# Kernel tuning notes

Measured on AMD Instinct MI355X. Metric: run time of the kernel, lower is better.

## Reference

```python
import jax, jax.numpy as jnp
import numpy as np

B, SQ, SK, D, H, DK, DV = 4, 2048, 2048, 1024, 16, 64, 64


def setup_inputs() -> dict:
    key = jax.random.key(0)
    ks = jax.random.split(key, 12)

    def xav(k, shape):
        fan_in, fan_out = shape[-2], shape[-1]
        lim = (6.0 / (fan_in + fan_out)) ** 0.5
        return jax.random.uniform(k, shape, jnp.float32, -lim, lim)

    return {
        "Q": jax.random.normal(ks[0], (B, SQ, D), jnp.float32),
        "K": jax.random.normal(ks[1], (B, SK, D), jnp.float32),
        "V": jax.random.normal(ks[2], (B, SK, D), jnp.float32),
        "padding_mask": jnp.zeros((B, 1, SK), jnp.bool_),
        "Wq": xav(ks[3], (H, D, DK)),
        "bq": jnp.zeros((H, DK), jnp.float32),
        "Wk": xav(ks[4], (H, D, DK)),
        "bk": jnp.zeros((H, DK), jnp.float32),
        "Wv": xav(ks[5], (H, D, DV)),
        "bv": jnp.zeros((H, DV), jnp.float32),
        "Wo": xav(ks[6], (H, DV, DV)),   # per-head Attention.linear
        "bo": jnp.zeros((H, DV), jnp.float32),
        "Wf": xav(ks[7], (H * DV, D)),   # final MultiHeadAttention.linear
        "bf": jnp.zeros((D,), jnp.float32),
    }


def reference(Q, K, V, padding_mask, Wq, bq, Wk, bk, Wv, bv, Wo, bo, Wf, bf):
    # Per-head projections, batched over heads instead of a python loop.
    q = jnp.einsum("bsd,hdk->bhsk", Q, Wq) + bq[:, None, :]  # [B,H,SQ,DK]
    k = jnp.einsum("bsd,hdk->bhsk", K, Wk) + bk[:, None, :]  # [B,H,SK,DK]
    v = jnp.einsum("bsd,hdv->bhsv", V, Wv) + bv[:, None, :]  # [B,H,SK,DV]

    scale = float(DK) ** 0.5
    w = jnp.einsum("bhqd,bhkd->bhqk", q, k) / scale           # [B,H,SQ,SK]

    causal = jnp.triu(jnp.ones((SQ, SK), jnp.bool_), 1)       # masking=True path
    w = jnp.where(causal[None, None], -jnp.inf, w)
    w = jnp.where(padding_mask[:, None, :, :], -jnp.inf, w)   # [B,1,1,SK]

    score = jnp.nan_to_num(jax.nn.softmax(w, axis=-1))        # nan_to_num as in torch
    # dropout p=0.0 -> identity
    ctx = jnp.einsum("bhqk,bhkv->bhqv", score, v)             # [B,H,SQ,DV]
    heads = jnp.einsum("bhqv,hvu->bhqu", ctx, Wo) + bo[:, None, :]
    concat = heads.transpose(0, 2, 1, 3).reshape(B, SQ, H * DV)
    return concat @ Wf + bf
```

## Files before the change

### kernel.cpp

```cpp
#include <hip/hip_runtime.h>

typedef unsigned short u16;
typedef __attribute__((ext_vector_type(8))) short short8;
typedef __attribute__((ext_vector_type(4))) float f32x4;

#define NEG (-1e30f)
#define SCL 0.180336880f

#define WS_WPQ   (0u)
#define WS_WPK   (2u<<20)
#define WS_WPV   (4u<<20)
#define WS_WBIG  (6u<<20)
#define WS_BC    (8u<<20)
#define WS_QB    (9u<<20)
#define WS_KB    (25u<<20)
#define WS_VB    (41u<<20)
#define WS_QP    (57u<<20)
#define WS_KP    (73u<<20)
#define WS_VP    (89u<<20)
#define WS_VT    (105u<<20)
#define WS_CTX   (121u<<20)

__device__ __forceinline__ u16 f2b(float f) {
    union { float f; unsigned u; } x; x.f = f;
    unsigned r = x.u + 0x7fffu + ((x.u >> 16) & 1u);
    return (u16)(r >> 16);
}

__device__ __forceinline__ void gload16(const void* g, void* lds) {
    __builtin_amdgcn_global_load_lds(
        (const __attribute__((address_space(1))) void*)g,
        (__attribute__((address_space(3))) void*)lds, 16, 0, 0);
}

__global__ __launch_bounds__(256) void conv_bf16(const float* __restrict__ in,
                                                 u16* __restrict__ out) {
    unsigned i = blockIdx.x * 256u + threadIdx.x;
    const float4* p = (const float4*)(in + (size_t)i * 8);
    float4 a = p[0], b = p[1];
    short8 o;
    o[0]=(short)f2b(a.x); o[1]=(short)f2b(a.y); o[2]=(short)f2b(a.z); o[3]=(short)f2b(a.w);
    o[4]=(short)f2b(b.x); o[5]=(short)f2b(b.y); o[6]=(short)f2b(b.z); o[7]=(short)f2b(b.w);
    *(short8*)(out + (size_t)i * 8) = o;
}

__global__ __launch_bounds__(256) void pack_qkv(const float* __restrict__ Wq,
                                                const float* __restrict__ Wk,
                                                const float* __restrict__ Wv,
                                                u16* __restrict__ pq,
                                                u16* __restrict__ pk,
                                                u16* __restrict__ pv) {
    unsigned idx = blockIdx.x * 256u + threadIdx.x;
    unsigned n = idx >> 10, d = idx & 1023u;
    unsigned h = n >> 6, kk = n & 63u;
    unsigned src = (h * 1024u + d) * 64u + kk;
    pq[idx] = f2b(Wq[src]);
    pk[idx] = f2b(Wk[src]);
    pv[idx] = f2b(Wv[src]);
}

__global__ __launch_bounds__(256) void make_wbig(const float* __restrict__ Wo,
                                                 const float* __restrict__ Wf,
                                                 u16* __restrict__ wbig) {
    unsigned idx = blockIdx.x * 256u + threadIdx.x;
    unsigned n = idx >> 10, k = idx & 1023u;
    unsigned h = k >> 6;
    float s = 0.f;
#pragma unroll 8
    for (int u = 0; u < 64; ++u)
        s += Wo[k * 64u + u] * Wf[(h * 64u + u) * 1024u + n];
    wbig[(size_t)n * 1024u + k] = f2b(s);
}

__global__ __launch_bounds__(256) void make_bcomb(const float* __restrict__ bo,
                                                  const float* __restrict__ bf,
                                                  const float* __restrict__ Wf,
                                                  float* __restrict__ bc) {
    __shared__ float red[16][17];
    const int tx = threadIdx.x & 15, ty = threadIdx.x >> 4;
    const int n = blockIdx.x * 16 + tx;
    float s = 0.f;
#pragma unroll
    for (int i = 0; i < 64; ++i) {
        int x = ty * 64 + i;
        s += bo[x] * Wf[(size_t)x * 1024 + n];
    }
    red[ty][tx] = s;
    __syncthreads();
    if (ty == 0) {
        float t = bf[n];
#pragma unroll
        for (int y = 0; y < 16; ++y) t += red[y][tx];
        bc[n] = t;
    }
}

__global__ __launch_bounds__(256) void vtrans(const u16* __restrict__ vp,
                                              u16* __restrict__ vt) {
    const int kvt = blockIdx.x, bh = blockIdx.y, b = bh >> 4, h = bh & 15;
    const int tid = threadIdx.x;
    __shared__ u16 T[64][72];
    {
        int kv_r = tid >> 2, dg = (tid & 3) * 16;
        const u16* src = vp + ((size_t)(b * 2048 + kvt * 64 + kv_r)) * 1024 + h * 64 + dg;
        short8 x0 = *(const short8*)src;
        short8 x1 = *(const short8*)(src + 8);
#pragma unroll
        for (int i = 0; i < 8; ++i) { T[dg + i][kv_r] = (u16)x0[i]; T[dg + 8 + i][kv_r] = (u16)x1[i]; }
    }
    __syncthreads();
    {
        int dv = tid >> 2, cg = (tid & 3) * 16;
        int swz = (dv & 7) << 3;
        u16* dst = vt + ((size_t)(bh * 64 + dv)) * 2048 + kvt * 64;
#pragma unroll
        for (int q = 0; q < 2; ++q) {
            int c0 = cg + q * 8;
            short8 y;
#pragma unroll
            for (int i = 0; i < 8; ++i) y[i] = (short)T[dv][c0 + i];
            *(short8*)(dst + (c0 ^ swz)) = y;
        }
    }
}

template <int OUT_BF16>
__global__ __launch_bounds__(256) void gemm_bf16(const u16* __restrict__ A,
                                                 const u16* __restrict__ Bt,
                                                 const float* __restrict__ bias,
                                                 void* __restrict__ Cv,
                                                 int M, int N, int K) {
    __shared__ __align__(16) u16 As[128 * 64];
    __shared__ __align__(16) u16 Bs[128 * 64];
    const int tid = threadIdx.x;
    const int lane = tid & 63, w = tid >> 6;
    const int li = lane & 15, g = lane >> 4;
    const int bm = blockIdx.y * 128, bn = blockIdx.x * 128;
    const int wm = w >> 1, wn = w & 1;

    f32x4 acc[4][4];
#pragma unroll
    for (int m = 0; m < 4; ++m)
#pragma unroll
        for (int n = 0; n < 4; ++n) acc[m][n] = (f32x4){0.f, 0.f, 0.f, 0.f};

    for (int k0 = 0; k0 < K; k0 += 64) {
        __syncthreads();
#pragma unroll
        for (int r = 0; r < 4; ++r) {
            int ch  = (r * 4 + w) * 64 + lane;
            int row = ch >> 3;
            int ck  = (ch & 7) ^ (row & 7);
            gload16(A  + (size_t)(bm + row) * K + k0 + ck * 8, (char*)As + (r * 4 + w) * 1024);
            gload16(Bt + (size_t)(bn + row) * K + k0 + ck * 8, (char*)Bs + (r * 4 + w) * 1024);
        }
        __syncthreads();
#pragma unroll
        for (int kk = 0; kk < 2; ++kk) {
            short8 a[4], b[4];
#pragma unroll
            for (int m = 0; m < 4; ++m) {
                int row = wm * 64 + m * 16 + li;
                int c = (kk * 4 + g) ^ (row & 7);
                a[m] = *(const short8*)(As + row * 64 + c * 8);
            }
#pragma unroll
            for (int n = 0; n < 4; ++n) {
                int row = wn * 64 + n * 16 + li;
                int c = (kk * 4 + g) ^ (row & 7);
                b[n] = *(const short8*)(Bs + row * 64 + c * 8);
            }
#pragma unroll
            for (int m = 0; m < 4; ++m)
#pragma unroll
                for (int n = 0; n < 4; ++n)
                    acc[m][n] = __builtin_amdgcn_mfma_f32_16x16x32_bf16(a[m], b[n], acc[m][n], 0, 0, 0);
        }
    }

#pragma unroll
    for (int n = 0; n < 4; ++n) {
        int col = bn + wn * 64 + n * 16 + li;
        float bv = bias[col];
#pragma unroll
        for (int m = 0; m < 4; ++m)
#pragma unroll
            for (int j = 0; j < 4; ++j) {
                int row = bm + wm * 64 + m * 16 + g * 4 + j;
                float v = acc[m][n][j] + bv;
                if (OUT_BF16) ((u16*)Cv)[(size_t)row * N + col] = f2b(v);
                else          ((float*)Cv)[(size_t)row * N + col] = v;
            }
    }
}

__global__ __launch_bounds__(256) void flash_attn(const u16* __restrict__ qp,
                                                  const u16* __restrict__ kp,
                                                  const u16* __restrict__ vt,
                                                  const unsigned char* __restrict__ pmask,
                                                  u16* __restrict__ ctx) {
    const int bh = blockIdx.x, b = bh >> 4, h = bh & 15;
    const int qt = 31 - blockIdx.y;
    const int tid = threadIdx.x, lane = tid & 63, w = tid >> 6;
    const int li = lane & 15, g = lane >> 4;

    __shared__ __align__(16) u16 Ks[2][64 * 64];
    __shared__ __align__(16) u16 Vs[2][64 * 64];
    __shared__ __align__(16) u16 Ps[64 * 64];

    auto STAGE = [&](int buf, int kt) {
#pragma unroll
        for (int r = 0; r < 2; ++r) {
            int ch  = (r * 4 + w) * 64 + lane;
            int row = ch >> 3, cc = ch & 7;
            int ck  = cc ^ (row & 7);
            gload16(kp + (size_t)(b * 2048 + kt * 64 + row) * 1024 + h * 64 + ck * 8,
                    (char*)(Ks[buf]) + (r * 4 + w) * 1024);
            gload16(vt + (size_t)(bh * 64 + row) * 2048 + kt * 64 + cc * 8,
                    (char*)(Vs[buf]) + (r * 4 + w) * 1024);
        }
    };

    STAGE(0, 0);
    const int rq = w * 16 + li;
    const u16* qg = qp + (size_t)(b * 2048 + qt * 64 + rq) * 1024 + h * 64;
    short8 aq0 = *(const short8*)(qg + g * 8);
    short8 aq1 = *(const short8*)(qg + 32 + g * 8);

    float m_i[4], l_i[4];
    f32x4 o_acc[4];
#pragma unroll
    for (int j = 0; j < 4; ++j) { m_i[j] = NEG; l_i[j] = 0.f; }
#pragma unroll
    for (int n = 0; n < 4; ++n) o_acc[n] = (f32x4){0.f, 0.f, 0.f, 0.f};

    const unsigned char* pm = pmask + (size_t)b * 2048;

    __syncthreads();
    int cur = 0;

    for (int kt = 0; kt <= qt; ++kt) {
        if (kt < qt) STAGE(cur ^ 1, kt + 1);

        f32x4 s[4];
#pragma unroll
        for (int n = 0; n < 4; ++n) s[n] = (f32x4){0.f, 0.f, 0.f, 0.f};
        __builtin_amdgcn_s_setprio(1);
#pragma unroll
        for (int kk = 0; kk < 2; ++kk) {
            short8 aq = kk ? aq1 : aq0;
#pragma unroll
            for (int n = 0; n < 4; ++n) {
                int rk = n * 16 + li;
                short8 bk = *(const short8*)(Ks[cur] + rk * 64 + (((kk * 4 + g) ^ (li & 7))) * 8);
                s[n] = __builtin_amdgcn_mfma_f32_16x16x32_bf16(aq, bk, s[n], 0, 0, 0);
            }
        }
        __builtin_amdgcn_s_setprio(0);

        float mcol[4];
#pragma unroll
        for (int n = 0; n < 4; ++n) mcol[n] = pm[kt * 64 + n * 16 + li] ? NEG : 0.f;
        const bool diag = (kt == qt);
        float rmax[4];
#pragma unroll
        for (int j = 0; j < 4; ++j) rmax[j] = NEG;
#pragma unroll
        for (int n = 0; n < 4; ++n) {
            int colk = kt * 64 + n * 16 + li;
#pragma unroll
            for (int j = 0; j < 4; ++j) {
                int rowq = qt * 64 + w * 16 + g * 4 + j;
                float v = s[n][j] * SCL + mcol[n];
                if (diag && colk > rowq) v = NEG;
                s[n][j] = v;
                rmax[j] = fmaxf(rmax[j], v);
            }
        }
#pragma unroll
        for (int off = 1; off < 16; off <<= 1)
#pragma unroll
            for (int j = 0; j < 4; ++j)
                rmax[j] = fmaxf(rmax[j], __shfl_xor(rmax[j], off));

        bool grow = (rmax[0] > m_i[0]) | (rmax[1] > m_i[1]) |
                    (rmax[2] > m_i[2]) | (rmax[3] > m_i[3]);
        if (__any(grow)) {
#pragma unroll
            for (int j = 0; j < 4; ++j) {
                float mn = fmaxf(m_i[j], rmax[j]);
                float a  = exp2f(m_i[j] - mn);
                m_i[j] = mn;
                l_i[j] *= a;
#pragma unroll
                for (int n = 0; n < 4; ++n) o_acc[n][j] *= a;
            }
        }

        float p[4][4], rsum[4] = {0.f, 0.f, 0.f, 0.f};
#pragma unroll
        for (int n = 0; n < 4; ++n)
#pragma unroll
            for (int j = 0; j < 4; ++j) {
                float pv = exp2f(s[n][j] - m_i[j]);
                p[n][j] = pv;
                rsum[j] += pv;
            }
#pragma unroll
        for (int off = 1; off < 16; off <<= 1)
#pragma unroll
            for (int j = 0; j < 4; ++j)
                rsum[j] += __shfl_xor(rsum[j], off);
#pragma unroll
        for (int j = 0; j < 4; ++j) l_i[j] += rsum[j];

#pragma unroll
        for (int j = 0; j < 4; ++j) {
            int rl  = g * 4 + j;
            int rg  = w * 16 + rl;
            int swz = (rl & 7) << 3;
#pragma unroll
            for (int n = 0; n < 4; ++n)
                Ps[rg * 64 + ((n * 16 + li) ^ swz)] = f2b(p[n][j]);
        }

        __builtin_amdgcn_s_setprio(1);
#pragma unroll
        for (int kk = 0; kk < 2; ++kk) {
            short8 pa = *(const short8*)(Ps + rq * 64 + (((kk * 4 + g) ^ (li & 7))) * 8);
#pragma unroll
            for (int n = 0; n < 4; ++n) {
                int rv = n * 16 + li;
                short8 vb = *(const short8*)(Vs[cur] + rv * 64 + (((kk * 4 + g) ^ (li & 7))) * 8);
                o_acc[n] = __builtin_amdgcn_mfma_f32_16x16x32_bf16(pa, vb, o_acc[n], 0, 0, 0);
            }
        }
        __builtin_amdgcn_s_setprio(0);

        __syncthreads();
        cur ^= 1;
    }

    float inv[4];
#pragma unroll
    for (int j = 0; j < 4; ++j) inv[j] = 1.f / l_i[j];
#pragma unroll
    for (int n = 0; n < 4; ++n)
#pragma unroll
        for (int j = 0; j < 4; ++j) {
            int rowq = qt * 64 + w * 16 + g * 4 + j;
            ctx[(size_t)(b * 2048 + rowq) * 1024 + h * 64 + n * 16 + li] = f2b(o_acc[n][j] * inv[j]);
        }
}

extern "C" void kernel_launch(void* const* d_in, const int* in_sizes, int n_in,
                              void* d_out, int out_size, void* d_ws, size_t ws_size,
                              hipStream_t stream) {
    const float* Q  = (const float*)d_in[0];
    const float* K  = (const float*)d_in[1];
    const float* V  = (const float*)d_in[2];
    const unsigned char* pmask = (const unsigned char*)d_in[3];
    const float* Wq = (const float*)d_in[4];
    const float* bq = (const float*)d_in[5];
    const float* Wk = (const float*)d_in[6];
    const float* bk = (const float*)d_in[7];
    const float* Wv = (const float*)d_in[8];
    const float* bv = (const float*)d_in[9];
    const float* Wo = (const float*)d_in[10];
    const float* bo = (const float*)d_in[11];
    const float* Wf = (const float*)d_in[12];
    const float* bf = (const float*)d_in[13];
    float* out = (float*)d_out;
    char*  ws  = (char*)d_ws;

    u16* WPQ = (u16*)(ws + WS_WPQ);  u16* WPK = (u16*)(ws + WS_WPK);
    u16* WPV = (u16*)(ws + WS_WPV);  u16* WBG = (u16*)(ws + WS_WBIG);
    float* BC = (float*)(ws + WS_BC);
    u16* QB = (u16*)(ws + WS_QB);  u16* KB = (u16*)(ws + WS_KB);  u16* VB = (u16*)(ws + WS_VB);
    u16* QP = (u16*)(ws + WS_QP);  u16* KP = (u16*)(ws + WS_KP);  u16* VP = (u16*)(ws + WS_VP);
    u16* VT = (u16*)(ws + WS_VT);  u16* CTX = (u16*)(ws + WS_CTX);

    conv_bf16<<<4096, 256, 0, stream>>>(Q, QB);
    conv_bf16<<<4096, 256, 0, stream>>>(K, KB);
    conv_bf16<<<4096, 256, 0, stream>>>(V, VB);
    pack_qkv<<<4096, 256, 0, stream>>>(Wq, Wk, Wv, WPQ, WPK, WPV);
    make_wbig<<<4096, 256, 0, stream>>>(Wo, Wf, WBG);
    make_bcomb<<<64, 256, 0, stream>>>(bo, bf, Wf, BC);

    dim3 g1(8, 64);
    gemm_bf16<1><<<g1, 256, 0, stream>>>(QB, WPQ, bq, QP, 8192, 1024, 1024);
    gemm_bf16<1><<<g1, 256, 0, stream>>>(KB, WPK, bk, KP, 8192, 1024, 1024);
    gemm_bf16<1><<<g1, 256, 0, stream>>>(VB, WPV, bv, VP, 8192, 1024, 1024);

    vtrans<<<dim3(32, 64), 256, 0, stream>>>(VP, VT);

    flash_attn<<<dim3(64, 32), 256, 0, stream>>>(QP, KP, VT, pmask, CTX);

    gemm_bf16<0><<<g1, 256, 0, stream>>>(CTX, WBG, BC, out, 8192, 1024, 1024);
}
```

Measured before the change: 471.7 us.

## Double-buffer GEMM, restructure flash attention softmax, and speed up weight preprocessing

The projection GEMM now double-buffers its LDS tiles so the next k-tile loads while the current one computes, and the softmax scale is folded into the Q projection epilogue. Flash attention swaps the MFMA operands so each lane owns a whole query row. This drops most cross-lane max and sum reductions, and P is packed with v_cvt_pk_bf16_f32. The padding mask becomes a precomputed float bias with a per-batch any-padded flag so unpadded batches skip mask loads, and the diagonal tile is peeled out of the loop. The weight pack and Wo·Wf combine kernels are rewritten with LDS tiling and coalesced accesses. The cost is doubled GEMM LDS use, which may lower occupancy.

```diff
diff --git a/kernel.cpp b/kernel.cpp
--- a/kernel.cpp
+++ b/kernel.cpp
@@ -1,6 +1,7 @@
 #include <hip/hip_runtime.h>
 
 typedef unsigned short u16;
+typedef unsigned int u32;
 typedef __attribute__((ext_vector_type(8))) short short8;
 typedef __attribute__((ext_vector_type(4))) float f32x4;
 
@@ -12,6 +13,8 @@
 #define WS_WPV   (4u<<20)
 #define WS_WBIG  (6u<<20)
 #define WS_BC    (8u<<20)
+#define WS_MB    ((8u<<20)+(1u<<16))
+#define WS_MP    ((8u<<20)+(3u<<16))
 #define WS_QB    (9u<<20)
 #define WS_KB    (25u<<20)
 #define WS_VB    (41u<<20)
@@ -25,6 +28,12 @@
     union { float f; unsigned u; } x; x.f = f;
     unsigned r = x.u + 0x7fffu + ((x.u >> 16) & 1u);
     return (u16)(r >> 16);
+}
+
+__device__ __forceinline__ u32 cvt_pk(float a, float b) {
+    u32 r;
+    asm("v_cvt_pk_bf16_f32 %0, %1, %2" : "=v"(r) : "v"(a), "v"(b));
+    return r;
 }
 
 __device__ __forceinline__ void gload16(const void* g, void* lds) {
@@ -50,32 +59,75 @@
                                                 u16* __restrict__ pq,
                                                 u16* __restrict__ pk,
                                                 u16* __restrict__ pv) {
-    unsigned idx = blockIdx.x * 256u + threadIdx.x;
-    unsigned n = idx >> 10, d = idx & 1023u;
-    unsigned h = n >> 6, kk = n & 63u;
-    unsigned src = (h * 1024u + d) * 64u + kk;
-    pq[idx] = f2b(Wq[src]);
-    pk[idx] = f2b(Wk[src]);
-    pv[idx] = f2b(Wv[src]);
+    __shared__ u16 T[64][68];
+    const int dt = blockIdx.x, h = blockIdx.y;
+    const int r = threadIdx.x >> 2, c0 = (threadIdx.x & 3) * 16;
+    const float* srcs[3] = {Wq, Wk, Wv};
+    u16* dsts[3] = {pq, pk, pv};
+#pragma unroll
+    for (int m = 0; m < 3; ++m) {
+        const float* src = srcs[m] + (size_t)(h * 1024 + dt * 64 + r) * 64 + c0;
+#pragma unroll
+        for (int i4 = 0; i4 < 4; ++i4) {
+            float4 x = *(const float4*)(src + i4 * 4);
+            T[c0 + i4*4 + 0][r] = f2b(x.x);
+            T[c0 + i4*4 + 1][r] = f2b(x.y);
+            T[c0 + i4*4 + 2][r] = f2b(x.z);
+            T[c0 + i4*4 + 3][r] = f2b(x.w);
+        }
+        __syncthreads();
+        u16* dst = dsts[m] + (size_t)(h * 64 + r) * 1024 + dt * 64 + c0;
+        short8 o0, o1;
+#pragma unroll
+        for (int i = 0; i < 8; ++i) { o0[i] = (short)T[r][c0 + i]; o1[i] = (short)T[r][c0 + 8 + i]; }
+        *(short8*)dst = o0;
+        *(short8*)(dst + 8) = o1;
+        __syncthreads();
+    }
 }
 
 __global__ __launch_bounds__(256) void make_wbig(const float* __restrict__ Wo,
                                                  const float* __restrict__ Wf,
                                                  u16* __restrict__ wbig) {
-    unsigned idx = blockIdx.x * 256u + threadIdx.x;
-    unsigned n = idx >> 10, k = idx & 1023u;
-    unsigned h = k >> 6;
-    float s = 0.f;
-#pragma unroll 8
+    __shared__ float WoL[64][64];
+    const int ct = blockIdx.x, h = blockIdx.y;
+    const int tid = threadIdx.x;
+#pragma unroll
+    for (int r = 0; r < 16; ++r) {
+        int i = r * 256 + tid;
+        WoL[i >> 6][i & 63] = Wo[h * 4096 + i];
+    }
+    __syncthreads();
+    const int n = ct * 256 + tid;
+    float wf[64];
+#pragma unroll
     for (int u = 0; u < 64; ++u)
-        s += Wo[k * 64u + u] * Wf[(h * 64u + u) * 1024u + n];
-    wbig[(size_t)n * 1024u + k] = f2b(s);
+        wf[u] = Wf[(size_t)(h * 64 + u) * 1024 + n];
+    u16* dst = wbig + (size_t)n * 1024 + h * 64;
+    for (int vb = 0; vb < 64; vb += 8) {
+        short8 o;
+#pragma unroll
+        for (int t = 0; t < 8; ++t) {
+            int v = vb + t;
+            float s = 0.f;
+#pragma unroll
+            for (int u4 = 0; u4 < 16; ++u4) {
+                float4 w4 = *(const float4*)&WoL[v][u4 * 4];
+                s += w4.x * wf[u4*4] + w4.y * wf[u4*4+1] + w4.z * wf[u4*4+2] + w4.w * wf[u4*4+3];
+            }
+            o[t] = (short)f2b(s);
+        }
+        *(short8*)(dst + vb) = o;
+    }
 }
 
 __global__ __launch_bounds__(256) void make_bcomb(const float* __restrict__ bo,
                                                   const float* __restrict__ bf,
                                                   const float* __restrict__ Wf,
-                                                  float* __restrict__ bc) {
+                                                  const unsigned char* __restrict__ pmask,
+                                                  float* __restrict__ bc,
+                                                  float* __restrict__ mbias,
+                                                  int* __restrict__ mpart) {
     __shared__ float red[16][17];
     const int tx = threadIdx.x & 15, ty = threadIdx.x >> 4;
     const int n = blockIdx.x * 16 + tx;
@@ -86,12 +138,21 @@
         s += bo[x] * Wf[(size_t)x * 1024 + n];
     }
     red[ty][tx] = s;
-    __syncthreads();
+
+    int t = blockIdx.x * 256 + threadIdx.x;
+    int v = 0;
+    if (t < 8192) {
+        v = pmask[t] ? 1 : 0;
+        mbias[t] = v ? NEG : 0.f;
+    }
+    int ba = __syncthreads_or(v);
+    if (threadIdx.x == 0 && blockIdx.x < 32) mpart[blockIdx.x] = ba;
+
     if (ty == 0) {
-        float t = bf[n];
-#pragma unroll
-        for (int y = 0; y < 16; ++y) t += red[y][tx];
-        bc[n] = t;
+        float tt = bf[n];
+#pragma unroll
+        for (int y = 0; y < 16; ++y) tt += red[y][tx];
+        bc[n] = tt;
     }
 }
 
@@ -129,32 +190,38 @@
                                                  const u16* __restrict__ Bt,
                                                  const float* __restrict__ bias,
                                                  void* __restrict__ Cv,
-                                                 int M, int N, int K) {
-    __shared__ __align__(16) u16 As[128 * 64];
-    __shared__ __align__(16) u16 Bs[128 * 64];
+                                                 int M, int N, int K, float oscale) {
+    __shared__ __align__(16) u16 As[2][128 * 64];
+    __shared__ __align__(16) u16 Bs[2][128 * 64];
     const int tid = threadIdx.x;
     const int lane = tid & 63, w = tid >> 6;
     const int li = lane & 15, g = lane >> 4;
     const int bm = blockIdx.y * 128, bn = blockIdx.x * 128;
     const int wm = w >> 1, wn = w & 1;
 
-    f32x4 acc[4][4];
-#pragma unroll
-    for (int m = 0; m < 4; ++m)
-#pragma unroll
-        for (int n = 0; n < 4; ++n) acc[m][n] = (f32x4){0.f, 0.f, 0.f, 0.f};
-
-    for (int k0 = 0; k0 < K; k0 += 64) {
-        __syncthreads();
+    auto STAGE = [&](int buf, int k0) {
 #pragma unroll
         for (int r = 0; r < 4; ++r) {
             int ch  = (r * 4 + w) * 64 + lane;
             int row = ch >> 3;
             int ck  = (ch & 7) ^ (row & 7);
-            gload16(A  + (size_t)(bm + row) * K + k0 + ck * 8, (char*)As + (r * 4 + w) * 1024);
-            gload16(Bt + (size_t)(bn + row) * K + k0 + ck * 8, (char*)Bs + (r * 4 + w) * 1024);
-        }
-        __syncthreads();
+            gload16(A  + (size_t)(bm + row) * K + k0 + ck * 8, (char*)(As[buf]) + (r * 4 + w) * 1024);
+            gload16(Bt + (size_t)(bn + row) * K + k0 + ck * 8, (char*)(Bs[buf]) + (r * 4 + w) * 1024);
+        }
+    };
+
+    f32x4 acc[4][4];
+#pragma unroll
+    for (int m = 0; m < 4; ++m)
+#pragma unroll
+        for (int n = 0; n < 4; ++n) acc[m][n] = (f32x4){0.f, 0.f, 0.f, 0.f};
+
+    STAGE(0, 0);
+    __syncthreads();
+    int cur = 0;
+
+    for (int k0 = 0; k0 < K; k0 += 64) {
+        if (k0 + 64 < K) STAGE(cur ^ 1, k0 + 64);
 #pragma unroll
         for (int kk = 0; kk < 2; ++kk) {
             short8 a[4], b[4];
@@ -162,13 +229,13 @@
             for (int m = 0; m < 4; ++m) {
                 int row = wm * 64 + m * 16 + li;
                 int c = (kk * 4 + g) ^ (row & 7);
-                a[m] = *(const short8*)(As + row * 64 + c * 8);
+                a[m] = *(const short8*)(As[cur] + row * 64 + c * 8);
             }
 #pragma unroll
             for (int n = 0; n < 4; ++n) {
                 int row = wn * 64 + n * 16 + li;
                 int c = (kk * 4 + g) ^ (row & 7);
-                b[n] = *(const short8*)(Bs + row * 64 + c * 8);
+                b[n] = *(const short8*)(Bs[cur] + row * 64 + c * 8);
             }
 #pragma unroll
             for (int m = 0; m < 4; ++m)
@@ -176,6 +243,8 @@
                 for (int n = 0; n < 4; ++n)
                     acc[m][n] = __builtin_amdgcn_mfma_f32_16x16x32_bf16(a[m], b[n], acc[m][n], 0, 0, 0);
         }
+        __syncthreads();
+        cur ^= 1;
     }
 
 #pragma unroll
@@ -187,7 +256,7 @@
 #pragma unroll
             for (int j = 0; j < 4; ++j) {
                 int row = bm + wm * 64 + m * 16 + g * 4 + j;
-                float v = acc[m][n][j] + bv;
+                float v = (acc[m][n][j] + bv) * oscale;
                 if (OUT_BF16) ((u16*)Cv)[(size_t)row * N + col] = f2b(v);
                 else          ((float*)Cv)[(size_t)row * N + col] = v;
             }
@@ -197,7 +266,8 @@
 __global__ __launch_bounds__(256) void flash_attn(const u16* __restrict__ qp,
                                                   const u16* __restrict__ kp,
                                                   const u16* __restrict__ vt,
-                                                  const unsigned char* __restrict__ pmask,
+                                                  const float* __restrict__ mbias,
+                                                  const int* __restrict__ mpart,
                                                   u16* __restrict__ ctx) {
     const int bh = blockIdx.x, b = bh >> 4, h = bh & 15;
     const int qt = 31 - blockIdx.y;
@@ -227,20 +297,32 @@
     short8 aq0 = *(const short8*)(qg + g * 8);
     short8 aq1 = *(const short8*)(qg + 32 + g * 8);
 
-    float m_i[4], l_i[4];
+    bool padded;
+    {
+        int a = 0;
+#pragma unroll
+        for (int i = 0; i < 8; ++i) a |= mpart[b * 8 + i];
+        padded = (a != 0);
+    }
+
+    float m_i = NEG, l_i = 0.f;
     f32x4 o_acc[4];
 #pragma unroll
-    for (int j = 0; j < 4; ++j) { m_i[j] = NEG; l_i[j] = 0.f; }
-#pragma unroll
     for (int n = 0; n < 4; ++n) o_acc[n] = (f32x4){0.f, 0.f, 0.f, 0.f};
 
-    const unsigned char* pm = pmask + (size_t)b * 2048;
+    const float* mb = mbias + (size_t)b * 2048;
+    const int swz = li & 7;
 
     __syncthreads();
     int cur = 0;
 
-    for (int kt = 0; kt <= qt; ++kt) {
-        if (kt < qt) STAGE(cur ^ 1, kt + 1);
+    auto TILE = [&](int kt, int buf, bool diag) {
+        float mcv[16];
+        if (padded) {
+#pragma unroll
+            for (int n = 0; n < 4; ++n)
+                *(float4*)(mcv + n * 4) = *(const float4*)(mb + kt * 64 + n * 16 + g * 4);
+        }
 
         f32x4 s[4];
 #pragma unroll
@@ -251,105 +333,87 @@
             short8 aq = kk ? aq1 : aq0;
 #pragma unroll
             for (int n = 0; n < 4; ++n) {
-                int rk = n * 16 + li;
-                short8 bk = *(const short8*)(Ks[cur] + rk * 64 + (((kk * 4 + g) ^ (li & 7))) * 8);
-                s[n] = __builtin_amdgcn_mfma_f32_16x16x32_bf16(aq, bk, s[n], 0, 0, 0);
+                short8 bk = *(const short8*)(Ks[buf] + (n * 16 + li) * 64 + ((kk * 4 + g) ^ swz) * 8);
+                s[n] = __builtin_amdgcn_mfma_f32_16x16x32_bf16(bk, aq, s[n], 0, 0, 0);
             }
         }
         __builtin_amdgcn_s_setprio(0);
 
-        float mcol[4];
-#pragma unroll
-        for (int n = 0; n < 4; ++n) mcol[n] = pm[kt * 64 + n * 16 + li] ? NEG : 0.f;
-        const bool diag = (kt == qt);
-        float rmax[4];
-#pragma unroll
-        for (int j = 0; j < 4; ++j) rmax[j] = NEG;
+        float rmax = NEG;
+#pragma unroll
+        for (int n = 0; n < 4; ++n)
+#pragma unroll
+            for (int j = 0; j < 4; ++j) {
+                float v = s[n][j];
+                if (padded) v += mcv[n * 4 + j];
+                if (diag && (n * 16 + g * 4 + j) > rq) v = NEG;
+                s[n][j] = v;
+                rmax = fmaxf(rmax, v);
+            }
+        rmax = fmaxf(rmax, __shfl_xor(rmax, 16));
+        rmax = fmaxf(rmax, __shfl_xor(rmax, 32));
+
+        if (__any(rmax > m_i)) {
+            float mn = fmaxf(m_i, rmax);
+            float a  = exp2f(m_i - mn);
+            m_i = mn;
+            l_i *= a;
+            float af[4];
+#pragma unroll
+            for (int j = 0; j < 4; ++j) af[j] = __shfl(a, g * 4 + j);
+#pragma unroll
+            for (int n = 0; n < 4; ++n)
+#pragma unroll
+                for (int j = 0; j < 4; ++j) o_acc[n][j] *= af[j];
+        }
+
+        float rs = 0.f;
 #pragma unroll
         for (int n = 0; n < 4; ++n) {
-            int colk = kt * 64 + n * 16 + li;
-#pragma unroll
-            for (int j = 0; j < 4; ++j) {
-                int rowq = qt * 64 + w * 16 + g * 4 + j;
-                float v = s[n][j] * SCL + mcol[n];
-                if (diag && colk > rowq) v = NEG;
-                s[n][j] = v;
-                rmax[j] = fmaxf(rmax[j], v);
-            }
-        }
-#pragma unroll
-        for (int off = 1; off < 16; off <<= 1)
-#pragma unroll
-            for (int j = 0; j < 4; ++j)
-                rmax[j] = fmaxf(rmax[j], __shfl_xor(rmax[j], off));
-
-        bool grow = (rmax[0] > m_i[0]) | (rmax[1] > m_i[1]) |
-                    (rmax[2] > m_i[2]) | (rmax[3] > m_i[3]);
-        if (__any(grow)) {
-#pragma unroll
-            for (int j = 0; j < 4; ++j) {
-                float mn = fmaxf(m_i[j], rmax[j]);
-                float a  = exp2f(m_i[j] - mn);
-                m_i[j] = mn;
-                l_i[j] *= a;
-#pragma unroll
-                for (int n = 0; n < 4; ++n) o_acc[n][j] *= a;
-            }
-        }
-
-        float p[4][4], rsum[4] = {0.f, 0.f, 0.f, 0.f};
-#pragma unroll
-        for (int n = 0; n < 4; ++n)
-#pragma unroll
-            for (int j = 0; j < 4; ++j) {
-                float pv = exp2f(s[n][j] - m_i[j]);
-                p[n][j] = pv;
-                rsum[j] += pv;
-            }
-#pragma unroll
-        for (int off = 1; off < 16; off <<= 1)
-#pragma unroll
-            for (int j = 0; j < 4; ++j)
-                rsum[j] += __shfl_xor(rsum[j], off);
-#pragma unroll
-        for (int j = 0; j < 4; ++j) l_i[j] += rsum[j];
-
-#pragma unroll
-        for (int j = 0; j < 4; ++j) {
-            int rl  = g * 4 + j;
-            int rg  = w * 16 + rl;
-            int swz = (rl & 7) << 3;
-#pragma unroll
-            for (int n = 0; n < 4; ++n)
-                Ps[rg * 64 + ((n * 16 + li) ^ swz)] = f2b(p[n][j]);
-        }
+            float p0 = exp2f(s[n][0] - m_i);
+            float p1 = exp2f(s[n][1] - m_i);
+            float p2 = exp2f(s[n][2] - m_i);
+            float p3 = exp2f(s[n][3] - m_i);
+            rs += (p0 + p1) + (p2 + p3);
+            u32 lo = cvt_pk(p0, p1), hi = cvt_pk(p2, p3);
+            int col = (n * 16 + g * 4) ^ (swz << 3);
+            *(uint2*)(Ps + rq * 64 + col) = make_uint2(lo, hi);
+        }
+        rs += __shfl_xor(rs, 16);
+        rs += __shfl_xor(rs, 32);
+        l_i += rs;
 
         __builtin_amdgcn_s_setprio(1);
 #pragma unroll
         for (int kk = 0; kk < 2; ++kk) {
-            short8 pa = *(const short8*)(Ps + rq * 64 + (((kk * 4 + g) ^ (li & 7))) * 8);
+            short8 pa = *(const short8*)(Ps + rq * 64 + ((kk * 4 + g) ^ swz) * 8);
 #pragma unroll
             for (int n = 0; n < 4; ++n) {
-                int rv = n * 16 + li;
-                short8 vb = *(const short8*)(Vs[cur] + rv * 64 + (((kk * 4 + g) ^ (li & 7))) * 8);
+                short8 vb = *(const short8*)(Vs[buf] + (n * 16 + li) * 64 + ((kk * 4 + g) ^ swz) * 8);
                 o_acc[n] = __builtin_amdgcn_mfma_f32_16x16x32_bf16(pa, vb, o_acc[n], 0, 0, 0);
             }
         }
         __builtin_amdgcn_s_setprio(0);
-
+    };
+
+    for (int kt = 0; kt < qt; ++kt) {
+        STAGE(cur ^ 1, kt + 1);
+        TILE(kt, cur, false);
         __syncthreads();
         cur ^= 1;
     }
-
-    float inv[4];
-#pragma unroll
-    for (int j = 0; j < 4; ++j) inv[j] = 1.f / l_i[j];
+    TILE(qt, cur, true);
+
+    float linv = 1.f / l_i;
+    float lr[4];
+#pragma unroll
+    for (int j = 0; j < 4; ++j) lr[j] = __shfl(linv, g * 4 + j);
 #pragma unroll
     for (int n = 0; n < 4; ++n)
 #pragma unroll
         for (int j = 0; j < 4; ++j) {
             int rowq = qt * 64 + w * 16 + g * 4 + j;
-            ctx[(size_t)(b * 2048 + rowq) * 1024 + h * 64 + n * 16 + li] = f2b(o_acc[n][j] * inv[j]);
+            ctx[(size_t)(b * 2048 + rowq) * 1024 + h * 64 + n * 16 + li] = f2b(o_acc[n][j] * lr[j]);
         }
 }
 
@@ -376,6 +440,8 @@
     u16* WPQ = (u16*)(ws + WS_WPQ);  u16* WPK = (u16*)(ws + WS_WPK);
     u16* WPV = (u16*)(ws + WS_WPV);  u16* WBG = (u16*)(ws + WS_WBIG);
     float* BC = (float*)(ws + WS_BC);
+    float* MB = (float*)(ws + WS_MB);
+    int*   MP = (int*)(ws + WS_MP);
     u16* QB = (u16*)(ws + WS_QB);  u16* KB = (u16*)(ws + WS_KB);  u16* VB = (u16*)(ws + WS_VB);
     u16* QP = (u16*)(ws + WS_QP);  u16* KP = (u16*)(ws + WS_KP);  u16* VP = (u16*)(ws + WS_VP);
     u16* VT = (u16*)(ws + WS_VT);  u16* CTX = (u16*)(ws + WS_CTX);
@@ -383,18 +449,18 @@
     conv_bf16<<<4096, 256, 0, stream>>>(Q, QB);
     conv_bf16<<<4096, 256, 0, stream>>>(K, KB);
     conv_bf16<<<4096, 256, 0, stream>>>(V, VB);
-    pack_qkv<<<4096, 256, 0, stream>>>(Wq, Wk, Wv, WPQ, WPK, WPV);
-    make_wbig<<<4096, 256, 0, stream>>>(Wo, Wf, WBG);
-    make_bcomb<<<64, 256, 0, stream>>>(bo, bf, Wf, BC);
+    pack_qkv<<<dim3(16, 16), 256, 0, stream>>>(Wq, Wk, Wv, WPQ, WPK, WPV);
+    make_wbig<<<dim3(4, 16), 256, 0, stream>>>(Wo, Wf, WBG);
+    make_bcomb<<<64, 256, 0, stream>>>(bo, bf, Wf, pmask, BC, MB, MP);
 
     dim3 g1(8, 64);
-    gemm_bf16<1><<<g1, 256, 0, stream>>>(QB, WPQ, bq, QP, 8192, 1024, 1024);
-    gemm_bf16<1><<<g1, 256, 0, stream>>>(KB, WPK, bk, KP, 8192, 1024, 1024);
-    gemm_bf16<1><<<g1, 256, 0, stream>>>(VB, WPV, bv, VP, 8192, 1024, 1024);
+    gemm_bf16<1><<<g1, 256, 0, stream>>>(QB, WPQ, bq, QP, 8192, 1024, 1024, SCL);
+    gemm_bf16<1><<<g1, 256, 0, stream>>>(KB, WPK, bk, KP, 8192, 1024, 1024, 1.0f);
+    gemm_bf16<1><<<g1, 256, 0, stream>>>(VB, WPV, bv, VP, 8192, 1024, 1024, 1.0f);
 
     vtrans<<<dim3(32, 64), 256, 0, stream>>>(VP, VT);
 
-    flash_attn<<<dim3(64, 32), 256, 0, stream>>>(QP, KP, VT, pmask, CTX);
-
-    gemm_bf16<0><<<g1, 256, 0, stream>>>(CTX, WBG, BC, out, 8192, 1024, 1024);
-}
+    flash_attn<<<dim3(64, 32), 256, 0, stream>>>(QP, KP, VT, MB, MP, CTX);
+
+    gemm_bf16<0><<<g1, 256, 0, stream>>>(CTX, WBG, BC, out, 8192, 1024, 1024, 1.0f);
+}
```

New measurement: 401.9 us. -14.8%, faster.
